# Performance work log

Hardware: AMD Instinct MI355X
Metric: run time of the kernel (lower is better)

## Reference

```python
import jax, jax.numpy as jnp
import numpy as np

N, E, D = 100000, 1600000, 128

def _sage_mean(x, src, dst, W_self, W_neigh, b, n_nodes):
    # mean over in-neighbors: sum messages by dst, divide by in-degree
    msg_sum = jax.ops.segment_sum(x[src], dst, num_segments=n_nodes)
    deg = jax.ops.segment_sum(jnp.ones((src.shape[0],), x.dtype), dst, num_segments=n_nodes)
    h_neigh = msg_sum / jnp.maximum(deg, 1.0)[:, None]
    # DGL SAGEConv (mean): fc_self(h) + fc_neigh(h_neigh) + bias
    return x @ W_self + h_neigh @ W_neigh + b

def setup_inputs() -> dict:
    key = jax.random.key(0)
    ks = jax.random.split(key, 9)
    s = 1.0 / np.sqrt(D)
    return {
        "x": jax.random.normal(ks[0], (N, D), jnp.float32),
        "src": jax.random.randint(ks[1], (E,), 0, N, jnp.int32),
        "dst": jax.random.randint(ks[2], (E,), 0, N, jnp.int32),
        "W_self1": jax.random.uniform(ks[3], (D, D), jnp.float32, -s, s),
        "W_neigh1": jax.random.uniform(ks[4], (D, D), jnp.float32, -s, s),
        "b1": jnp.zeros((D,), jnp.float32),
        "W_self2": jax.random.uniform(ks[5], (D, D), jnp.float32, -s, s),
        "W_neigh2": jax.random.uniform(ks[6], (D, D), jnp.float32, -s, s),
        "b2": jnp.zeros((D,), jnp.float32),
    }

def reference(x, src, dst, W_self1, W_neigh1, b1, W_self2, W_neigh2, b2):
    n = x.shape[0]
    h = jax.nn.relu(_sage_mean(x, src, dst, W_self1, W_neigh1, b1, n))
    h = jax.nn.relu(_sage_mean(h, src, dst, W_self2, W_neigh2, b2, n))
    return h
```

## Files before the change

### kernel.cpp

```cpp
#include <hip/hip_runtime.h>

#define DF 128

typedef __bf16 bf16x8_t __attribute__((ext_vector_type(8)));
typedef float f32x4_t __attribute__((ext_vector_type(4)));
typedef float f32x2_t __attribute__((ext_vector_type(2)));
typedef unsigned short ushort_t;
typedef ushort_t ushort8_t __attribute__((ext_vector_type(8)));

static __device__ __forceinline__ ushort_t f2bf(float f) {
    union { float f; unsigned int u; } v; v.f = f;
    unsigned int r = v.u + 0x7fffu + ((v.u >> 16) & 1u);
    return (ushort_t)(r >> 16);
}
static __device__ __forceinline__ float bf2f(ushort_t v) {
    union { unsigned int u; float f; } c; c.u = ((unsigned int)v) << 16; return c.f;
}

__global__ __launch_bounds__(256) void k1_coarse_hist(
    const int* __restrict__ dst, int* __restrict__ C,
    int E, int CH, int NCH, int NBKT) {
    __shared__ int lcnt[512];
    const int c = blockIdx.x;
    for (int b = threadIdx.x; b < NBKT; b += 256) lcnt[b] = 0;
    __syncthreads();
    const int base = c * CH, lim = min(base + CH, E);
    for (int i = base + threadIdx.x; i < lim; i += 256)
        atomicAdd(&lcnt[dst[i] >> 8], 1);
    __syncthreads();
    for (int b = threadIdx.x; b < NBKT; b += 256) C[b * NCH + c] = lcnt[b];
}

__global__ __launch_bounds__(512) void k2a_row_scan(
    int* __restrict__ C, int* __restrict__ rowtot, int NCH) {
    __shared__ int sd[512];
    const int b = blockIdx.x, t = threadIdx.x;
    int v = (t < NCH) ? C[b * NCH + t] : 0;
    sd[t] = v; __syncthreads();
    for (int off = 1; off < 512; off <<= 1) {
        int u = (t >= off) ? sd[t - off] : 0;
        __syncthreads();
        sd[t] += u;
        __syncthreads();
    }
    if (t < NCH) C[b * NCH + t] = sd[t] - v;
    if (t == 511) rowtot[b] = sd[511];
}

__global__ __launch_bounds__(512) void k2b_base_scan(
    const int* __restrict__ rowtot, int* __restrict__ rowbase,
    int* __restrict__ rowptr, int NBKT, int N, int E) {
    __shared__ int sd[512];
    const int t = threadIdx.x;
    int v = (t < NBKT) ? rowtot[t] : 0;
    sd[t] = v; __syncthreads();
    for (int off = 1; off < 512; off <<= 1) {
        int u = (t >= off) ? sd[t - off] : 0;
        __syncthreads();
        sd[t] += u;
        __syncthreads();
    }
    if (t < NBKT) rowbase[t] = sd[t] - v;
    if (t == 0) { rowbase[NBKT] = E; rowptr[N] = E; }
}

__global__ __launch_bounds__(256) void k3_bin_scatter(
    const int* __restrict__ src, const int* __restrict__ dst,
    const int* __restrict__ C, const int* __restrict__ rowbase,
    unsigned int* __restrict__ inter, int E, int CH, int NCH, int NBKT) {
    __shared__ int cur[512];
    const int c = blockIdx.x;
    for (int b = threadIdx.x; b < NBKT; b += 256)
        cur[b] = rowbase[b] + C[b * NCH + c];
    __syncthreads();
    const int base = c * CH, lim = min(base + CH, E);
    for (int i = base + threadIdx.x; i < lim; i += 256) {
        int d = dst[i];
        int s = src[i];
        int pos = atomicAdd(&cur[d >> 8], 1);
        inter[pos] = ((unsigned int)(d & 255) << 24) | (unsigned int)s;
    }
}

#define K4CAP 6144
__global__ __launch_bounds__(256) void k4_fine_scatter(
    const unsigned int* __restrict__ inter, const int* __restrict__ rowbase,
    int* __restrict__ edge_src, int* __restrict__ rowptr, int N) {
    __shared__ unsigned int stage[K4CAP];
    __shared__ unsigned int outv[K4CAP];
    __shared__ int lcnt[256], lofs[256], lrun[256];
    const int b = blockIdx.x, t = threadIdx.x;
    const int base = rowbase[b], count = rowbase[b + 1] - base;
    const int n0 = b << 8;
    const int nn = min(256, N - n0);

    lcnt[t] = 0; lrun[t] = 0;
    __syncthreads();

    if (count <= K4CAP) {
        for (int i = t; i < count; i += 256) {
            unsigned int v = inter[base + i];
            stage[i] = v;
            atomicAdd(&lcnt[v >> 24], 1);
        }
        __syncthreads();
        int cv = lcnt[t];
        lofs[t] = cv; __syncthreads();
        for (int off = 1; off < 256; off <<= 1) {
            int u = (t >= off) ? lofs[t - off] : 0;
            __syncthreads();
            lofs[t] += u;
            __syncthreads();
        }
        lofs[t] -= cv;
        if (t < nn) rowptr[n0 + t] = base + lofs[t];
        __syncthreads();
        for (int i = t; i < count; i += 256) {
            unsigned int v = stage[i];
            int dl = v >> 24;
            int p = lofs[dl] + atomicAdd(&lrun[dl], 1);
            outv[p] = v & 0xFFFFFFu;
        }
        __syncthreads();
        for (int i = t; i < count; i += 256) edge_src[base + i] = (int)outv[i];
    } else {
        for (int i = t; i < count; i += 256)
            atomicAdd(&lcnt[inter[base + i] >> 24], 1);
        __syncthreads();
        int cv = lcnt[t];
        lofs[t] = cv; __syncthreads();
        for (int off = 1; off < 256; off <<= 1) {
            int u = (t >= off) ? lofs[t - off] : 0;
            __syncthreads();
            lofs[t] += u;
            __syncthreads();
        }
        lofs[t] -= cv;
        if (t < nn) rowptr[n0 + t] = base + lofs[t];
        __syncthreads();
        for (int i = t; i < count; i += 256) {
            unsigned int v = inter[base + i];
            int dl = v >> 24;
            int p = atomicAdd(&lrun[dl], 1);
            edge_src[base + lofs[dl] + p] = (int)(v & 0xFFFFFFu);
        }
    }
}

__global__ __launch_bounds__(256) void conv_dual_kernel(
    const float* __restrict__ in, ushort_t* __restrict__ outb,
    unsigned char* __restrict__ out8, int n8) {
    int i = blockIdx.x * blockDim.x + threadIdx.x;
    if (i >= n8) return;
    float4 a = ((const float4*)in)[(size_t)i * 2];
    float4 b = ((const float4*)in)[(size_t)i * 2 + 1];
    ushort8_t o;
    o[0] = f2bf(a.x); o[1] = f2bf(a.y); o[2] = f2bf(a.z); o[3] = f2bf(a.w);
    o[4] = f2bf(b.x); o[5] = f2bf(b.y); o[6] = f2bf(b.z); o[7] = f2bf(b.w);
    ((ushort8_t*)outb)[i] = o;
    int lo = __builtin_amdgcn_cvt_pk_fp8_f32(a.x, a.y, 0, false);
    lo     = __builtin_amdgcn_cvt_pk_fp8_f32(a.z, a.w, lo, true);
    int hi = __builtin_amdgcn_cvt_pk_fp8_f32(b.x, b.y, 0, false);
    hi     = __builtin_amdgcn_cvt_pk_fp8_f32(b.z, b.w, hi, true);
    ((uint2*)out8)[i] = make_uint2((unsigned int)lo, (unsigned int)hi);
}

__global__ __launch_bounds__(256) void conv_b2f8_kernel(
    const ushort_t* __restrict__ in, unsigned char* __restrict__ out8, int n8) {
    int i = blockIdx.x * blockDim.x + threadIdx.x;
    if (i >= n8) return;
    ushort8_t v = ((const ushort8_t*)in)[i];
    int lo = __builtin_amdgcn_cvt_pk_fp8_f32(bf2f(v[0]), bf2f(v[1]), 0, false);
    lo     = __builtin_amdgcn_cvt_pk_fp8_f32(bf2f(v[2]), bf2f(v[3]), lo, true);
    int hi = __builtin_amdgcn_cvt_pk_fp8_f32(bf2f(v[4]), bf2f(v[5]), 0, false);
    hi     = __builtin_amdgcn_cvt_pk_fp8_f32(bf2f(v[6]), bf2f(v[7]), hi, true);
    ((uint2*)out8)[i] = make_uint2((unsigned int)lo, (unsigned int)hi);
}

__global__ void transpose_w_kernel(const float* __restrict__ W0, const float* __restrict__ W1,
                                   const float* __restrict__ W2, const float* __restrict__ W3,
                                   ushort_t* __restrict__ out) {
    int m = blockIdx.x >> 6;
    const float* W = (m == 0) ? W0 : (m == 1) ? W1 : (m == 2) ? W2 : W3;
    int idx = (blockIdx.x & 63) * 256 + threadIdx.x;
    int k = idx >> 7, n = idx & 127;
    out[m * 16384 + n * 128 + k] = f2bf(W[idx]);
}

__global__ __launch_bounds__(256, 4) void aggregate_fp8_kernel(
    const unsigned char* __restrict__ Xf8, const int* __restrict__ rowptr,
    const int* __restrict__ edge_src, ushort_t* __restrict__ out, int N) {
    int node = (int)((blockIdx.x * 256u + threadIdx.x) >> 6);
    int lane = threadIdx.x & 63;
    if (node >= N) return;
    const int g = lane >> 4;
    const int s = lane & 15;
    int beg = rowptr[node], end = rowptr[node + 1];
    int deg = end - beg;
    f32x2_t ac0 = {0.f, 0.f}, ac1 = {0.f, 0.f}, ac2 = {0.f, 0.f}, ac3 = {0.f, 0.f};
    for (int b0 = 0; b0 < deg; b0 += 64) {
        int nb = min(64, deg - b0);
        int idx = (lane < nb) ? edge_src[beg + b0 + lane] : 0;
        int nfull = nb >> 4;
        for (int it = 0; it < nfull; ++it) {
            int j = it * 16 + g * 4;
            int s0 = __shfl(idx, j, 64);
            int s1 = __shfl(idx, j + 1, 64);
            int s2 = __shfl(idx, j + 2, 64);
            int s3 = __shfl(idx, j + 3, 64);
            uint2 v0 = *(const uint2*)(Xf8 + (size_t)s0 * DF + s * 8);
            uint2 v1 = *(const uint2*)(Xf8 + (size_t)s1 * DF + s * 8);
            uint2 v2 = *(const uint2*)(Xf8 + (size_t)s2 * DF + s * 8);
            uint2 v3 = *(const uint2*)(Xf8 + (size_t)s3 * DF + s * 8);
            ac0 += __builtin_amdgcn_cvt_pk_f32_fp8((int)v0.x, false);
            ac1 += __builtin_amdgcn_cvt_pk_f32_fp8((int)v0.x, true);
            ac2 += __builtin_amdgcn_cvt_pk_f32_fp8((int)v0.y, false);
            ac3 += __builtin_amdgcn_cvt_pk_f32_fp8((int)v0.y, true);
            ac0 += __builtin_amdgcn_cvt_pk_f32_fp8((int)v1.x, false);
            ac1 += __builtin_amdgcn_cvt_pk_f32_fp8((int)v1.x, true);
            ac2 += __builtin_amdgcn_cvt_pk_f32_fp8((int)v1.y, false);
            ac3 += __builtin_amdgcn_cvt_pk_f32_fp8((int)v1.y, true);
            ac0 += __builtin_amdgcn_cvt_pk_f32_fp8((int)v2.x, false);
            ac1 += __builtin_amdgcn_cvt_pk_f32_fp8((int)v2.x, true);
            ac2 += __builtin_amdgcn_cvt_pk_f32_fp8((int)v2.y, false);
            ac3 += __builtin_amdgcn_cvt_pk_f32_fp8((int)v2.y, true);
            ac0 += __builtin_amdgcn_cvt_pk_f32_fp8((int)v3.x, false);
            ac1 += __builtin_amdgcn_cvt_pk_f32_fp8((int)v3.x, true);
            ac2 += __builtin_amdgcn_cvt_pk_f32_fp8((int)v3.y, false);
            ac3 += __builtin_amdgcn_cvt_pk_f32_fp8((int)v3.y, true);
        }
        if (nb & 15) {
            int j = nfull * 16 + g * 4;
            int j0 = j, j1 = j + 1, j2 = j + 2, j3 = j + 3;
            int s0 = __shfl(idx, (j0 < nb) ? j0 : 0, 64);
            int s1 = __shfl(idx, (j1 < nb) ? j1 : 0, 64);
            int s2 = __shfl(idx, (j2 < nb) ? j2 : 0, 64);
            int s3 = __shfl(idx, (j3 < nb) ? j3 : 0, 64);
            uint2 z = make_uint2(0, 0);
            uint2 v0 = z, v1 = z, v2 = z, v3 = z;
            if (j0 < nb) v0 = *(const uint2*)(Xf8 + (size_t)s0 * DF + s * 8);
            if (j1 < nb) v1 = *(const uint2*)(Xf8 + (size_t)s1 * DF + s * 8);
            if (j2 < nb) v2 = *(const uint2*)(Xf8 + (size_t)s2 * DF + s * 8);
            if (j3 < nb) v3 = *(const uint2*)(Xf8 + (size_t)s3 * DF + s * 8);
            ac0 += __builtin_amdgcn_cvt_pk_f32_fp8((int)v0.x, false);
            ac1 += __builtin_amdgcn_cvt_pk_f32_fp8((int)v0.x, true);
            ac2 += __builtin_amdgcn_cvt_pk_f32_fp8((int)v0.y, false);
            ac3 += __builtin_amdgcn_cvt_pk_f32_fp8((int)v0.y, true);
            ac0 += __builtin_amdgcn_cvt_pk_f32_fp8((int)v1.x, false);
            ac1 += __builtin_amdgcn_cvt_pk_f32_fp8((int)v1.x, true);
            ac2 += __builtin_amdgcn_cvt_pk_f32_fp8((int)v1.y, false);
            ac3 += __builtin_amdgcn_cvt_pk_f32_fp8((int)v1.y, true);
            ac0 += __builtin_amdgcn_cvt_pk_f32_fp8((int)v2.x, false);
            ac1 += __builtin_amdgcn_cvt_pk_f32_fp8((int)v2.x, true);
            ac2 += __builtin_amdgcn_cvt_pk_f32_fp8((int)v2.y, false);
            ac3 += __builtin_amdgcn_cvt_pk_f32_fp8((int)v2.y, true);
            ac0 += __builtin_amdgcn_cvt_pk_f32_fp8((int)v3.x, false);
            ac1 += __builtin_amdgcn_cvt_pk_f32_fp8((int)v3.x, true);
            ac2 += __builtin_amdgcn_cvt_pk_f32_fp8((int)v3.y, false);
            ac3 += __builtin_amdgcn_cvt_pk_f32_fp8((int)v3.y, true);
        }
    }
    float r[8] = {ac0[0], ac0[1], ac1[0], ac1[1], ac2[0], ac2[1], ac3[0], ac3[1]};
#pragma unroll
    for (int i = 0; i < 8; ++i) {
        r[i] += __shfl_xor(r[i], 16, 64);
        r[i] += __shfl_xor(r[i], 32, 64);
    }
    if (g == 0) {
        float inv = 1.0f / fmaxf((float)deg, 1.0f);
        ushort8_t o;
#pragma unroll
        for (int i = 0; i < 8; ++i) o[i] = f2bf(r[i] * inv);
        *(ushort8_t*)(out + (size_t)node * DF + s * 8) = o;
    }
}

template <int BF16OUT>
__global__ __launch_bounds__(256, 2) void sage_mfma_kernel(
    const ushort_t* Xb, const ushort_t* __restrict__ Ab,
    const ushort_t* __restrict__ Wts, const ushort_t* __restrict__ Wtn,
    const float* __restrict__ bias, void* outv, int M) {
    __shared__ ushort_t sW[32768];

    const int lane = threadIdx.x & 63;
    const int w = threadIdx.x >> 6;
    const int l15 = lane & 15;
    const int g = lane >> 4;
    const int m0 = blockIdx.x * 128 + w * 32;

    int r0 = m0 + l15;      if (r0 >= M) r0 = M - 1;
    int r1 = m0 + 16 + l15; if (r1 >= M) r1 = M - 1;

    for (int u = threadIdx.x; u < 4096; u += 256) {
        int row = u >> 4;
        int kb  = (u & 15) << 4;
        int swz = kb ^ ((row & 7) << 4);
        const ushort_t* gp = (row < 128)
            ? (Wts + ((size_t)row << 7) + (kb >> 1))
            : (Wtn + ((size_t)(row - 128) << 7) + (kb >> 1));
        *(ushort8_t*)((char*)sW + row * 256 + swz) = *(const ushort8_t*)gp;
    }

    bf16x8_t a[2][2][4];
#pragma unroll
    for (int mat = 0; mat < 2; ++mat) {
        const ushort_t* As = mat ? Ab : Xb;
#pragma unroll
        for (int ks = 0; ks < 4; ++ks) {
            const int ko = ks * 32 + g * 8;
            a[mat][0][ks] = *(const bf16x8_t*)(As + (size_t)r0 * DF + ko);
            a[mat][1][ks] = *(const bf16x8_t*)(As + (size_t)r1 * DF + ko);
        }
    }

    __syncthreads();

    f32x4_t acc[2][8];
#pragma unroll
    for (int rf = 0; rf < 2; ++rf)
#pragma unroll
        for (int c = 0; c < 8; ++c) acc[rf][c] = (f32x4_t){0.f, 0.f, 0.f, 0.f};

#pragma unroll
    for (int mat = 0; mat < 2; ++mat) {
#pragma unroll
        for (int ks = 0; ks < 4; ++ks) {
            const int kb = ks * 64 + g * 16;
#pragma unroll
            for (int c = 0; c < 8; ++c) {
                int brow = mat * 128 + c * 16 + l15;
                bf16x8_t b = *(const bf16x8_t*)((const char*)sW + brow * 256 +
                                                (kb ^ ((brow & 7) << 4)));
                acc[0][c] = __builtin_amdgcn_mfma_f32_16x16x32_bf16(a[mat][0][ks], b, acc[0][c], 0, 0, 0);
                acc[1][c] = __builtin_amdgcn_mfma_f32_16x16x32_bf16(a[mat][1][ks], b, acc[1][c], 0, 0, 0);
            }
        }
    }

    if (m0 + 32 <= M) {
#pragma unroll
        for (int c = 0; c < 8; ++c) {
            int col = c * 16 + l15;
            float bv = bias[col];
#pragma unroll
            for (int rf = 0; rf < 2; ++rf)
#pragma unroll
                for (int j = 0; j < 4; ++j) {
                    int row = m0 + rf * 16 + g * 4 + j;
                    float v = fmaxf(acc[rf][c][j] + bv, 0.f);
                    if (BF16OUT) ((ushort_t*)outv)[(size_t)row * DF + col] = f2bf(v);
                    else         ((float*)outv)[(size_t)row * DF + col] = v;
                }
        }
    } else {
#pragma unroll
        for (int c = 0; c < 8; ++c) {
            int col = c * 16 + l15;
            float bv = bias[col];
#pragma unroll
            for (int rf = 0; rf < 2; ++rf)
#pragma unroll
                for (int j = 0; j < 4; ++j) {
                    int row = m0 + rf * 16 + g * 4 + j;
                    if (row < M) {
                        float v = fmaxf(acc[rf][c][j] + bv, 0.f);
                        if (BF16OUT) ((ushort_t*)outv)[(size_t)row * DF + col] = f2bf(v);
                        else         ((float*)outv)[(size_t)row * DF + col] = v;
                    }
                }
        }
    }
}

extern "C" void kernel_launch(void* const* d_in, const int* in_sizes, int n_in,
                              void* d_out, int out_size, void* d_ws, size_t ws_size,
                              hipStream_t stream) {
    const int N = in_sizes[0] / DF;
    const int E = in_sizes[1];

    const float* x   = (const float*)d_in[0];
    const int*   src = (const int*)d_in[1];
    const int*   dst = (const int*)d_in[2];
    const float* Ws1 = (const float*)d_in[3];
    const float* Wn1 = (const float*)d_in[4];
    const float* b1  = (const float*)d_in[5];
    const float* Ws2 = (const float*)d_in[6];
    const float* Wn2 = (const float*)d_in[7];
    const float* b2  = (const float*)d_in[8];
    float* out = (float*)d_out;

    const int NBKT = (N + 255) >> 8;
    int CH = 4096;
    int NCH = (E + CH - 1) / CH;
    while (NCH > 512) { CH <<= 1; NCH = (E + CH - 1) / CH; }

    int* rowptr   = (int*)d_ws;
    int* rowbase  = rowptr + ((N + 1 + 63) & ~63);
    int* rowtot   = rowbase + ((NBKT + 1 + 63) & ~63);
    int* C        = rowtot + ((NBKT + 63) & ~63);
    ushort_t* Wt  = (ushort_t*)(C + ((NBKT * NCH + 63) & ~63));
    int* edge_src = (int*)(Wt + 65536);
    ushort_t* Xb  = (ushort_t*)(edge_src + ((E + 63) & ~63));
    ushort_t* Ab  = Xb + (size_t)N * DF;
    unsigned int* inter = (unsigned int*)Ab;

    unsigned char* Xf8  = (unsigned char*)d_out;
    unsigned char* H1f8 = Xf8 + (size_t)N * DF;

    conv_dual_kernel<<<(N * DF / 8 + 255) / 256, 256, 0, stream>>>(x, Xb, Xf8, N * DF / 8);
    k1_coarse_hist<<<NCH, 256, 0, stream>>>(dst, C, E, CH, NCH, NBKT);
    k2a_row_scan<<<NBKT, 512, 0, stream>>>(C, rowtot, NCH);
    k2b_base_scan<<<1, 512, 0, stream>>>(rowtot, rowbase, rowptr, NBKT, N, E);
    k3_bin_scatter<<<NCH, 256, 0, stream>>>(src, dst, C, rowbase, inter, E, CH, NCH, NBKT);
    k4_fine_scatter<<<NBKT, 256, 0, stream>>>(inter, rowbase, edge_src, rowptr, N);
    transpose_w_kernel<<<256, 256, 0, stream>>>(Ws1, Wn1, Ws2, Wn2, Wt);

    const int aggGrid  = (N + 3) / 4;
    const int gemmGrid = (N + 127) / 128;

    aggregate_fp8_kernel<<<aggGrid, 256, 0, stream>>>(Xf8, rowptr, edge_src, Ab, N);
    sage_mfma_kernel<1><<<gemmGrid, 256, 0, stream>>>(Xb, Ab, Wt, Wt + 16384, b1, (void*)Xb, N);
    conv_b2f8_kernel<<<(N * DF / 8 + 255) / 256, 256, 0, stream>>>(Xb, H1f8, N * DF / 8);
    aggregate_fp8_kernel<<<aggGrid, 256, 0, stream>>>(H1f8, rowptr, edge_src, Ab, N);
    sage_mfma_kernel<0><<<gemmGrid, 256, 0, stream>>>(Xb, Ab, Wt + 32768, Wt + 49152, b2, (void*)out, N);
}
```

Baseline: 196.7 us.

## Fuse FP8 conversion into layer-1 GEMM epilogue and simplify aggregation loop

```diff
diff --git a/kernel.cpp b/kernel.cpp
--- a/kernel.cpp
+++ b/kernel.cpp
@@ -12,9 +12,6 @@
     union { float f; unsigned int u; } v; v.f = f;
     unsigned int r = v.u + 0x7fffu + ((v.u >> 16) & 1u);
     return (ushort_t)(r >> 16);
-}
-static __device__ __forceinline__ float bf2f(ushort_t v) {
-    union { unsigned int u; float f; } c; c.u = ((unsigned int)v) << 16; return c.f;
 }
 
 __global__ __launch_bounds__(256) void k1_coarse_hist(
@@ -165,18 +162,6 @@
     ((uint2*)out8)[i] = make_uint2((unsigned int)lo, (unsigned int)hi);
 }
 
-__global__ __launch_bounds__(256) void conv_b2f8_kernel(
-    const ushort_t* __restrict__ in, unsigned char* __restrict__ out8, int n8) {
-    int i = blockIdx.x * blockDim.x + threadIdx.x;
-    if (i >= n8) return;
-    ushort8_t v = ((const ushort8_t*)in)[i];
-    int lo = __builtin_amdgcn_cvt_pk_fp8_f32(bf2f(v[0]), bf2f(v[1]), 0, false);
-    lo     = __builtin_amdgcn_cvt_pk_fp8_f32(bf2f(v[2]), bf2f(v[3]), lo, true);
-    int hi = __builtin_amdgcn_cvt_pk_fp8_f32(bf2f(v[4]), bf2f(v[5]), 0, false);
-    hi     = __builtin_amdgcn_cvt_pk_fp8_f32(bf2f(v[6]), bf2f(v[7]), hi, true);
-    ((uint2*)out8)[i] = make_uint2((unsigned int)lo, (unsigned int)hi);
-}
-
 __global__ void transpose_w_kernel(const float* __restrict__ W0, const float* __restrict__ W1,
                                    const float* __restrict__ W2, const float* __restrict__ W3,
                                    ushort_t* __restrict__ out) {
@@ -195,70 +180,37 @@
     if (node >= N) return;
     const int g = lane >> 4;
     const int s = lane & 15;
-    int beg = rowptr[node], end = rowptr[node + 1];
-    int deg = end - beg;
+    const int beg = rowptr[node], end = rowptr[node + 1];
+    const int deg = end - beg;
     f32x2_t ac0 = {0.f, 0.f}, ac1 = {0.f, 0.f}, ac2 = {0.f, 0.f}, ac3 = {0.f, 0.f};
-    for (int b0 = 0; b0 < deg; b0 += 64) {
-        int nb = min(64, deg - b0);
-        int idx = (lane < nb) ? edge_src[beg + b0 + lane] : 0;
-        int nfull = nb >> 4;
-        for (int it = 0; it < nfull; ++it) {
-            int j = it * 16 + g * 4;
-            int s0 = __shfl(idx, j, 64);
-            int s1 = __shfl(idx, j + 1, 64);
-            int s2 = __shfl(idx, j + 2, 64);
-            int s3 = __shfl(idx, j + 3, 64);
-            uint2 v0 = *(const uint2*)(Xf8 + (size_t)s0 * DF + s * 8);
-            uint2 v1 = *(const uint2*)(Xf8 + (size_t)s1 * DF + s * 8);
-            uint2 v2 = *(const uint2*)(Xf8 + (size_t)s2 * DF + s * 8);
-            uint2 v3 = *(const uint2*)(Xf8 + (size_t)s3 * DF + s * 8);
-            ac0 += __builtin_amdgcn_cvt_pk_f32_fp8((int)v0.x, false);
-            ac1 += __builtin_amdgcn_cvt_pk_f32_fp8((int)v0.x, true);
-            ac2 += __builtin_amdgcn_cvt_pk_f32_fp8((int)v0.y, false);
-            ac3 += __builtin_amdgcn_cvt_pk_f32_fp8((int)v0.y, true);
-            ac0 += __builtin_amdgcn_cvt_pk_f32_fp8((int)v1.x, false);
-            ac1 += __builtin_amdgcn_cvt_pk_f32_fp8((int)v1.x, true);
-            ac2 += __builtin_amdgcn_cvt_pk_f32_fp8((int)v1.y, false);
-            ac3 += __builtin_amdgcn_cvt_pk_f32_fp8((int)v1.y, true);
-            ac0 += __builtin_amdgcn_cvt_pk_f32_fp8((int)v2.x, false);
-            ac1 += __builtin_amdgcn_cvt_pk_f32_fp8((int)v2.x, true);
-            ac2 += __builtin_amdgcn_cvt_pk_f32_fp8((int)v2.y, false);
-            ac3 += __builtin_amdgcn_cvt_pk_f32_fp8((int)v2.y, true);
-            ac0 += __builtin_amdgcn_cvt_pk_f32_fp8((int)v3.x, false);
-            ac1 += __builtin_amdgcn_cvt_pk_f32_fp8((int)v3.x, true);
-            ac2 += __builtin_amdgcn_cvt_pk_f32_fp8((int)v3.y, false);
-            ac3 += __builtin_amdgcn_cvt_pk_f32_fp8((int)v3.y, true);
-        }
-        if (nb & 15) {
-            int j = nfull * 16 + g * 4;
-            int j0 = j, j1 = j + 1, j2 = j + 2, j3 = j + 3;
-            int s0 = __shfl(idx, (j0 < nb) ? j0 : 0, 64);
-            int s1 = __shfl(idx, (j1 < nb) ? j1 : 0, 64);
-            int s2 = __shfl(idx, (j2 < nb) ? j2 : 0, 64);
-            int s3 = __shfl(idx, (j3 < nb) ? j3 : 0, 64);
-            uint2 z = make_uint2(0, 0);
-            uint2 v0 = z, v1 = z, v2 = z, v3 = z;
-            if (j0 < nb) v0 = *(const uint2*)(Xf8 + (size_t)s0 * DF + s * 8);
-            if (j1 < nb) v1 = *(const uint2*)(Xf8 + (size_t)s1 * DF + s * 8);
-            if (j2 < nb) v2 = *(const uint2*)(Xf8 + (size_t)s2 * DF + s * 8);
-            if (j3 < nb) v3 = *(const uint2*)(Xf8 + (size_t)s3 * DF + s * 8);
-            ac0 += __builtin_amdgcn_cvt_pk_f32_fp8((int)v0.x, false);
-            ac1 += __builtin_amdgcn_cvt_pk_f32_fp8((int)v0.x, true);
-            ac2 += __builtin_amdgcn_cvt_pk_f32_fp8((int)v0.y, false);
-            ac3 += __builtin_amdgcn_cvt_pk_f32_fp8((int)v0.y, true);
-            ac0 += __builtin_amdgcn_cvt_pk_f32_fp8((int)v1.x, false);
-            ac1 += __builtin_amdgcn_cvt_pk_f32_fp8((int)v1.x, true);
-            ac2 += __builtin_amdgcn_cvt_pk_f32_fp8((int)v1.y, false);
-            ac3 += __builtin_amdgcn_cvt_pk_f32_fp8((int)v1.y, true);
-            ac0 += __builtin_amdgcn_cvt_pk_f32_fp8((int)v2.x, false);
-            ac1 += __builtin_amdgcn_cvt_pk_f32_fp8((int)v2.x, true);
-            ac2 += __builtin_amdgcn_cvt_pk_f32_fp8((int)v2.y, false);
-            ac3 += __builtin_amdgcn_cvt_pk_f32_fp8((int)v2.y, true);
-            ac0 += __builtin_amdgcn_cvt_pk_f32_fp8((int)v3.x, false);
-            ac1 += __builtin_amdgcn_cvt_pk_f32_fp8((int)v3.x, true);
-            ac2 += __builtin_amdgcn_cvt_pk_f32_fp8((int)v3.y, false);
-            ac3 += __builtin_amdgcn_cvt_pk_f32_fp8((int)v3.y, true);
-        }
+    for (int e0 = beg + g * 4; e0 < end; e0 += 16) {
+        int i0 = edge_src[e0];
+        int i1 = edge_src[e0 + 1];
+        int i2 = edge_src[e0 + 2];
+        int i3 = edge_src[e0 + 3];
+        int rem = end - e0;
+        uint2 z = make_uint2(0u, 0u);
+        uint2 v0 = *(const uint2*)(Xf8 + (size_t)i0 * DF + s * 8);
+        uint2 v1 = z, v2 = z, v3 = z;
+        if (rem > 1) v1 = *(const uint2*)(Xf8 + (size_t)i1 * DF + s * 8);
+        if (rem > 2) v2 = *(const uint2*)(Xf8 + (size_t)i2 * DF + s * 8);
+        if (rem > 3) v3 = *(const uint2*)(Xf8 + (size_t)i3 * DF + s * 8);
+        ac0 += __builtin_amdgcn_cvt_pk_f32_fp8((int)v0.x, false);
+        ac1 += __builtin_amdgcn_cvt_pk_f32_fp8((int)v0.x, true);
+        ac2 += __builtin_amdgcn_cvt_pk_f32_fp8((int)v0.y, false);
+        ac3 += __builtin_amdgcn_cvt_pk_f32_fp8((int)v0.y, true);
+        ac0 += __builtin_amdgcn_cvt_pk_f32_fp8((int)v1.x, false);
+        ac1 += __builtin_amdgcn_cvt_pk_f32_fp8((int)v1.x, true);
+        ac2 += __builtin_amdgcn_cvt_pk_f32_fp8((int)v1.y, false);
+        ac3 += __builtin_amdgcn_cvt_pk_f32_fp8((int)v1.y, true);
+        ac0 += __builtin_amdgcn_cvt_pk_f32_fp8((int)v2.x, false);
+        ac1 += __builtin_amdgcn_cvt_pk_f32_fp8((int)v2.x, true);
+        ac2 += __builtin_amdgcn_cvt_pk_f32_fp8((int)v2.y, false);
+        ac3 += __builtin_amdgcn_cvt_pk_f32_fp8((int)v2.y, true);
+        ac0 += __builtin_amdgcn_cvt_pk_f32_fp8((int)v3.x, false);
+        ac1 += __builtin_amdgcn_cvt_pk_f32_fp8((int)v3.x, true);
+        ac2 += __builtin_amdgcn_cvt_pk_f32_fp8((int)v3.y, false);
+        ac3 += __builtin_amdgcn_cvt_pk_f32_fp8((int)v3.y, true);
     }
     float r[8] = {ac0[0], ac0[1], ac1[0], ac1[1], ac2[0], ac2[1], ac3[0], ac3[1]};
 #pragma unroll
@@ -279,7 +231,8 @@
 __global__ __launch_bounds__(256, 2) void sage_mfma_kernel(
     const ushort_t* Xb, const ushort_t* __restrict__ Ab,
     const ushort_t* __restrict__ Wts, const ushort_t* __restrict__ Wtn,
-    const float* __restrict__ bias, void* outv, int M) {
+    const float* __restrict__ bias, void* outv, unsigned char* __restrict__ out8,
+    int M) {
     __shared__ ushort_t sW[32768];
 
     const int lane = threadIdx.x & 63;
@@ -337,38 +290,26 @@
         }
     }
 
-    if (m0 + 32 <= M) {
-#pragma unroll
-        for (int c = 0; c < 8; ++c) {
-            int col = c * 16 + l15;
-            float bv = bias[col];
-#pragma unroll
-            for (int rf = 0; rf < 2; ++rf)
-#pragma unroll
-                for (int j = 0; j < 4; ++j) {
-                    int row = m0 + rf * 16 + g * 4 + j;
+#pragma unroll
+    for (int c = 0; c < 8; ++c) {
+        int col = c * 16 + l15;
+        float bv = bias[col];
+#pragma unroll
+        for (int rf = 0; rf < 2; ++rf)
+#pragma unroll
+            for (int j = 0; j < 4; ++j) {
+                int row = m0 + rf * 16 + g * 4 + j;
+                if (row < M) {
                     float v = fmaxf(acc[rf][c][j] + bv, 0.f);
-                    if (BF16OUT) ((ushort_t*)outv)[(size_t)row * DF + col] = f2bf(v);
-                    else         ((float*)outv)[(size_t)row * DF + col] = v;
-                }
-        }
-    } else {
-#pragma unroll
-        for (int c = 0; c < 8; ++c) {
-            int col = c * 16 + l15;
-            float bv = bias[col];
-#pragma unroll
-            for (int rf = 0; rf < 2; ++rf)
-#pragma unroll
-                for (int j = 0; j < 4; ++j) {
-                    int row = m0 + rf * 16 + g * 4 + j;
-                    if (row < M) {
-                        float v = fmaxf(acc[rf][c][j] + bv, 0.f);
-                        if (BF16OUT) ((ushort_t*)outv)[(size_t)row * DF + col] = f2bf(v);
-                        else         ((float*)outv)[(size_t)row * DF + col] = v;
+                    if (BF16OUT) {
+                        ((ushort_t*)outv)[(size_t)row * DF + col] = f2bf(v);
+                        int p = __builtin_amdgcn_cvt_pk_fp8_f32(v, v, 0, false);
+                        out8[(size_t)row * DF + col] = (unsigned char)(p & 0xff);
+                    } else {
+                        ((float*)outv)[(size_t)row * DF + col] = v;
                     }
                 }
-        }
+            }
     }
 }
 
@@ -400,7 +341,7 @@
     int* C        = rowtot + ((NBKT + 63) & ~63);
     ushort_t* Wt  = (ushort_t*)(C + ((NBKT * NCH + 63) & ~63));
     int* edge_src = (int*)(Wt + 65536);
-    ushort_t* Xb  = (ushort_t*)(edge_src + ((E + 63) & ~63));
+    ushort_t* Xb  = (ushort_t*)(edge_src + ((E + 64 + 63) & ~63));
     ushort_t* Ab  = Xb + (size_t)N * DF;
     unsigned int* inter = (unsigned int*)Ab;
 
@@ -419,8 +360,9 @@
     const int gemmGrid = (N + 127) / 128;
 
     aggregate_fp8_kernel<<<aggGrid, 256, 0, stream>>>(Xf8, rowptr, edge_src, Ab, N);
-    sage_mfma_kernel<1><<<gemmGrid, 256, 0, stream>>>(Xb, Ab, Wt, Wt + 16384, b1, (void*)Xb, N);
-    conv_b2f8_kernel<<<(N * DF / 8 + 255) / 256, 256, 0, stream>>>(Xb, H1f8, N * DF / 8);
+    sage_mfma_kernel<1><<<gemmGrid, 256, 0, stream>>>(Xb, Ab, Wt, Wt + 16384, b1,
+                                                      (void*)Xb, H1f8, N);
     aggregate_fp8_kernel<<<aggGrid, 256, 0, stream>>>(H1f8, rowptr, edge_src, Ab, N);
-    sage_mfma_kernel<0><<<gemmGrid, 256, 0, stream>>>(Xb, Ab, Wt + 32768, Wt + 49152, b2, (void*)out, N);
-}
+    sage_mfma_kernel<0><<<gemmGrid, 256, 0, stream>>>(Xb, Ab, Wt + 32768, Wt + 49152, b2,
+                                                      (void*)out, nullptr, N);
+}
```

Result: slower. 234.9 us (+19.4%).

## Merge prep kernels into one launch and halve GEMM shared memory

Applied to the files above, without the earlier changes.

```diff
diff --git a/kernel.cpp b/kernel.cpp
--- a/kernel.cpp
+++ b/kernel.cpp
@@ -17,18 +17,47 @@
     union { unsigned int u; float f; } c; c.u = ((unsigned int)v) << 16; return c.f;
 }
 
-__global__ __launch_bounds__(256) void k1_coarse_hist(
+__global__ __launch_bounds__(256) void prep_kernel(
+    const float* __restrict__ x, ushort_t* __restrict__ Xb,
+    unsigned char* __restrict__ Xf8, int n8, int nConv,
     const int* __restrict__ dst, int* __restrict__ C,
-    int E, int CH, int NCH, int NBKT) {
+    int E, int CH, int NCH, int NBKT,
+    const float* __restrict__ W0, const float* __restrict__ W1,
+    const float* __restrict__ W2, const float* __restrict__ W3,
+    ushort_t* __restrict__ Wt) {
     __shared__ int lcnt[512];
-    const int c = blockIdx.x;
-    for (int b = threadIdx.x; b < NBKT; b += 256) lcnt[b] = 0;
-    __syncthreads();
-    const int base = c * CH, lim = min(base + CH, E);
-    for (int i = base + threadIdx.x; i < lim; i += 256)
-        atomicAdd(&lcnt[dst[i] >> 8], 1);
-    __syncthreads();
-    for (int b = threadIdx.x; b < NBKT; b += 256) C[b * NCH + c] = lcnt[b];
+    const int b = blockIdx.x;
+    if (b < nConv) {
+        int i = b * 256 + threadIdx.x;
+        if (i >= n8) return;
+        float4 a = ((const float4*)x)[(size_t)i * 2];
+        float4 c4 = ((const float4*)x)[(size_t)i * 2 + 1];
+        ushort8_t o;
+        o[0] = f2bf(a.x); o[1] = f2bf(a.y); o[2] = f2bf(a.z); o[3] = f2bf(a.w);
+        o[4] = f2bf(c4.x); o[5] = f2bf(c4.y); o[6] = f2bf(c4.z); o[7] = f2bf(c4.w);
+        ((ushort8_t*)Xb)[i] = o;
+        int lo = __builtin_amdgcn_cvt_pk_fp8_f32(a.x, a.y, 0, false);
+        lo     = __builtin_amdgcn_cvt_pk_fp8_f32(a.z, a.w, lo, true);
+        int hi = __builtin_amdgcn_cvt_pk_fp8_f32(c4.x, c4.y, 0, false);
+        hi     = __builtin_amdgcn_cvt_pk_fp8_f32(c4.z, c4.w, hi, true);
+        ((uint2*)Xf8)[i] = make_uint2((unsigned int)lo, (unsigned int)hi);
+    } else if (b < nConv + NCH) {
+        const int c = b - nConv;
+        for (int k = threadIdx.x; k < NBKT; k += 256) lcnt[k] = 0;
+        __syncthreads();
+        const int base = c * CH, lim = min(base + CH, E);
+        for (int i = base + threadIdx.x; i < lim; i += 256)
+            atomicAdd(&lcnt[dst[i] >> 8], 1);
+        __syncthreads();
+        for (int k = threadIdx.x; k < NBKT; k += 256) C[k * NCH + c] = lcnt[k];
+    } else {
+        const int tb = b - nConv - NCH;
+        int m = tb >> 6;
+        const float* W = (m == 0) ? W0 : (m == 1) ? W1 : (m == 2) ? W2 : W3;
+        int idx = (tb & 63) * 256 + threadIdx.x;
+        int k = idx >> 7, n = idx & 127;
+        Wt[m * 16384 + n * 128 + k] = f2bf(W[idx]);
+    }
 }
 
 __global__ __launch_bounds__(512) void k2a_row_scan(
@@ -147,24 +176,6 @@
     }
 }
 
-__global__ __launch_bounds__(256) void conv_dual_kernel(
-    const float* __restrict__ in, ushort_t* __restrict__ outb,
-    unsigned char* __restrict__ out8, int n8) {
-    int i = blockIdx.x * blockDim.x + threadIdx.x;
-    if (i >= n8) return;
-    float4 a = ((const float4*)in)[(size_t)i * 2];
-    float4 b = ((const float4*)in)[(size_t)i * 2 + 1];
-    ushort8_t o;
-    o[0] = f2bf(a.x); o[1] = f2bf(a.y); o[2] = f2bf(a.z); o[3] = f2bf(a.w);
-    o[4] = f2bf(b.x); o[5] = f2bf(b.y); o[6] = f2bf(b.z); o[7] = f2bf(b.w);
-    ((ushort8_t*)outb)[i] = o;
-    int lo = __builtin_amdgcn_cvt_pk_fp8_f32(a.x, a.y, 0, false);
-    lo     = __builtin_amdgcn_cvt_pk_fp8_f32(a.z, a.w, lo, true);
-    int hi = __builtin_amdgcn_cvt_pk_fp8_f32(b.x, b.y, 0, false);
-    hi     = __builtin_amdgcn_cvt_pk_fp8_f32(b.z, b.w, hi, true);
-    ((uint2*)out8)[i] = make_uint2((unsigned int)lo, (unsigned int)hi);
-}
-
 __global__ __launch_bounds__(256) void conv_b2f8_kernel(
     const ushort_t* __restrict__ in, unsigned char* __restrict__ out8, int n8) {
     int i = blockIdx.x * blockDim.x + threadIdx.x;
@@ -175,16 +186,6 @@
     int hi = __builtin_amdgcn_cvt_pk_fp8_f32(bf2f(v[4]), bf2f(v[5]), 0, false);
     hi     = __builtin_amdgcn_cvt_pk_fp8_f32(bf2f(v[6]), bf2f(v[7]), hi, true);
     ((uint2*)out8)[i] = make_uint2((unsigned int)lo, (unsigned int)hi);
-}
-
-__global__ void transpose_w_kernel(const float* __restrict__ W0, const float* __restrict__ W1,
-                                   const float* __restrict__ W2, const float* __restrict__ W3,
-                                   ushort_t* __restrict__ out) {
-    int m = blockIdx.x >> 6;
-    const float* W = (m == 0) ? W0 : (m == 1) ? W1 : (m == 2) ? W2 : W3;
-    int idx = (blockIdx.x & 63) * 256 + threadIdx.x;
-    int k = idx >> 7, n = idx & 127;
-    out[m * 16384 + n * 128 + k] = f2bf(W[idx]);
 }
 
 __global__ __launch_bounds__(256, 4) void aggregate_fp8_kernel(
@@ -276,11 +277,11 @@
 }
 
 template <int BF16OUT>
-__global__ __launch_bounds__(256, 2) void sage_mfma_kernel(
+__global__ __launch_bounds__(256, 3) void sage_mfma_kernel(
     const ushort_t* Xb, const ushort_t* __restrict__ Ab,
     const ushort_t* __restrict__ Wts, const ushort_t* __restrict__ Wtn,
     const float* __restrict__ bias, void* outv, int M) {
-    __shared__ ushort_t sW[32768];
+    __shared__ ushort_t sW[16384];
 
     const int lane = threadIdx.x & 63;
     const int w = threadIdx.x >> 6;
@@ -291,14 +292,12 @@
     int r0 = m0 + l15;      if (r0 >= M) r0 = M - 1;
     int r1 = m0 + 16 + l15; if (r1 >= M) r1 = M - 1;
 
-    for (int u = threadIdx.x; u < 4096; u += 256) {
+    for (int u = threadIdx.x; u < 2048; u += 256) {
         int row = u >> 4;
         int kb  = (u & 15) << 4;
         int swz = kb ^ ((row & 7) << 4);
-        const ushort_t* gp = (row < 128)
-            ? (Wts + ((size_t)row << 7) + (kb >> 1))
-            : (Wtn + ((size_t)(row - 128) << 7) + (kb >> 1));
-        *(ushort8_t*)((char*)sW + row * 256 + swz) = *(const ushort8_t*)gp;
+        *(ushort8_t*)((char*)sW + row * 256 + swz) =
+            *(const ushort8_t*)(Wts + ((size_t)row << 7) + (kb >> 1));
     }
 
     bf16x8_t a[2][2][4];
@@ -313,27 +312,46 @@
         }
     }
 
+    f32x4_t acc[2][8];
+#pragma unroll
+    for (int rf = 0; rf < 2; ++rf)
+#pragma unroll
+        for (int c = 0; c < 8; ++c) acc[rf][c] = (f32x4_t){0.f, 0.f, 0.f, 0.f};
+
     __syncthreads();
-
-    f32x4_t acc[2][8];
-#pragma unroll
-    for (int rf = 0; rf < 2; ++rf)
-#pragma unroll
-        for (int c = 0; c < 8; ++c) acc[rf][c] = (f32x4_t){0.f, 0.f, 0.f, 0.f};
-
-#pragma unroll
-    for (int mat = 0; mat < 2; ++mat) {
-#pragma unroll
-        for (int ks = 0; ks < 4; ++ks) {
-            const int kb = ks * 64 + g * 16;
-#pragma unroll
-            for (int c = 0; c < 8; ++c) {
-                int brow = mat * 128 + c * 16 + l15;
-                bf16x8_t b = *(const bf16x8_t*)((const char*)sW + brow * 256 +
-                                                (kb ^ ((brow & 7) << 4)));
-                acc[0][c] = __builtin_amdgcn_mfma_f32_16x16x32_bf16(a[mat][0][ks], b, acc[0][c], 0, 0, 0);
-                acc[1][c] = __builtin_amdgcn_mfma_f32_16x16x32_bf16(a[mat][1][ks], b, acc[1][c], 0, 0, 0);
-            }
+#pragma unroll
+    for (int ks = 0; ks < 4; ++ks) {
+        const int kb = ks * 64 + g * 16;
+#pragma unroll
+        for (int c = 0; c < 8; ++c) {
+            int brow = c * 16 + l15;
+            bf16x8_t b = *(const bf16x8_t*)((const char*)sW + brow * 256 +
+                                            (kb ^ ((brow & 7) << 4)));
+            acc[0][c] = __builtin_amdgcn_mfma_f32_16x16x32_bf16(a[0][0][ks], b, acc[0][c], 0, 0, 0);
+            acc[1][c] = __builtin_amdgcn_mfma_f32_16x16x32_bf16(a[0][1][ks], b, acc[1][c], 0, 0, 0);
+        }
+    }
+    __syncthreads();
+
+    for (int u = threadIdx.x; u < 2048; u += 256) {
+        int row = u >> 4;
+        int kb  = (u & 15) << 4;
+        int swz = kb ^ ((row & 7) << 4);
+        *(ushort8_t*)((char*)sW + row * 256 + swz) =
+            *(const ushort8_t*)(Wtn + ((size_t)row << 7) + (kb >> 1));
+    }
+    __syncthreads();
+
+#pragma unroll
+    for (int ks = 0; ks < 4; ++ks) {
+        const int kb = ks * 64 + g * 16;
+#pragma unroll
+        for (int c = 0; c < 8; ++c) {
+            int brow = c * 16 + l15;
+            bf16x8_t b = *(const bf16x8_t*)((const char*)sW + brow * 256 +
+                                            (kb ^ ((brow & 7) << 4)));
+            acc[0][c] = __builtin_amdgcn_mfma_f32_16x16x32_bf16(a[1][0][ks], b, acc[0][c], 0, 0, 0);
+            acc[1][c] = __builtin_amdgcn_mfma_f32_16x16x32_bf16(a[1][1][ks], b, acc[1][c], 0, 0, 0);
         }
     }
 
@@ -400,27 +418,30 @@
     int* C        = rowtot + ((NBKT + 63) & ~63);
     ushort_t* Wt  = (ushort_t*)(C + ((NBKT * NCH + 63) & ~63));
     int* edge_src = (int*)(Wt + 65536);
-    ushort_t* Xb  = (ushort_t*)(edge_src + ((E + 63) & ~63));
+    ushort_t* Xb  = (ushort_t*)(edge_src + ((E + 64 + 63) & ~63));
     ushort_t* Ab  = Xb + (size_t)N * DF;
     unsigned int* inter = (unsigned int*)Ab;
 
     unsigned char* Xf8  = (unsigned char*)d_out;
     unsigned char* H1f8 = Xf8 + (size_t)N * DF;
 
-    conv_dual_kernel<<<(N * DF / 8 + 255) / 256, 256, 0, stream>>>(x, Xb, Xf8, N * DF / 8);
-    k1_coarse_hist<<<NCH, 256, 0, stream>>>(dst, C, E, CH, NCH, NBKT);
+    const int n8 = N * DF / 8;
+    const int nConv = (n8 + 255) / 256;
+
+    prep_kernel<<<nConv + NCH + 256, 256, 0, stream>>>(
+        x, Xb, Xf8, n8, nConv, dst, C, E, CH, NCH, NBKT,
+        Ws1, Wn1, Ws2, Wn2, Wt);
     k2a_row_scan<<<NBKT, 512, 0, stream>>>(C, rowtot, NCH);
     k2b_base_scan<<<1, 512, 0, stream>>>(rowtot, rowbase, rowptr, NBKT, N, E);
     k3_bin_scatter<<<NCH, 256, 0, stream>>>(src, dst, C, rowbase, inter, E, CH, NCH, NBKT);
     k4_fine_scatter<<<NBKT, 256, 0, stream>>>(inter, rowbase, edge_src, rowptr, N);
-    transpose_w_kernel<<<256, 256, 0, stream>>>(Ws1, Wn1, Ws2, Wn2, Wt);
 
     const int aggGrid  = (N + 3) / 4;
     const int gemmGrid = (N + 127) / 128;
 
     aggregate_fp8_kernel<<<aggGrid, 256, 0, stream>>>(Xf8, rowptr, edge_src, Ab, N);
     sage_mfma_kernel<1><<<gemmGrid, 256, 0, stream>>>(Xb, Ab, Wt, Wt + 16384, b1, (void*)Xb, N);
-    conv_b2f8_kernel<<<(N * DF / 8 + 255) / 256, 256, 0, stream>>>(Xb, H1f8, N * DF / 8);
+    conv_b2f8_kernel<<<(n8 + 255) / 256, 256, 0, stream>>>(Xb, H1f8, n8);
     aggregate_fp8_kernel<<<aggGrid, 256, 0, stream>>>(H1f8, rowptr, edge_src, Ab, N);
     sage_mfma_kernel<0><<<gemmGrid, 256, 0, stream>>>(Xb, Ab, Wt + 32768, Wt + 49152, b2, (void*)out, N);
 }
```

Result: faster. 184.3 us (-6.3%).
